# Kernel tuning notes

Measured on AMD Instinct MI355X. Metric: run time of the kernel, lower is better.

## Reference

```python
import jax, jax.numpy as jnp
import numpy as np

N = 50000      # entities
R = 400        # relations
D = 300        # init/hidden/output dim (hard-coded 300 in module)
E = 800000     # edges over N+R nodes
B = 2048       # aligned train pairs
L = 32         # padded neighbor sequence length
H, DK = 8, 32  # n_head=8, d_k=d_v=32
GAMMA1, GAMMA2 = 0.9, 0.2


def setup_inputs() -> dict:
    key = jax.random.key(0)
    ks = iter(jax.random.split(key, 48))
    nk = lambda: next(ks)
    inp = {}
    inp["e_x"] = jax.random.normal(nk(), (N, D), jnp.float32)
    inp["r_x"] = jax.random.normal(nk(), (R, 2 * D), jnp.float32)
    inp["edge_w"] = jax.random.uniform(nk(), (E,), jnp.float32)
    # learned params (fan-in scaled)
    s = lambda fi: 1.0 / np.sqrt(fi)
    inp["Wrel"] = jax.random.normal(nk(), (2 * D, D), jnp.float32) * s(2 * D)
    inp["brel"] = jnp.zeros((D,), jnp.float32)
    inp["W1"] = jax.random.normal(nk(), (D, D), jnp.float32) * s(D)
    inp["b1"] = jnp.zeros((D,), jnp.float32)
    inp["W2"] = jax.random.normal(nk(), (D, D), jnp.float32) * s(D)
    inp["b2"] = jnp.zeros((D,), jnp.float32)
    inp["Wprox"] = jax.random.normal(nk(), (2 * D, D), jnp.float32) * s(2 * D)
    inp["bprox"] = jnp.zeros((D,), jnp.float32)
    # encoder params, index 0 = input_encoder, 1 = output_encoder
    inp["enc_Wq"] = jax.random.normal(nk(), (2, D, H * DK), jnp.float32) * s(D)
    inp["enc_Wk"] = jax.random.normal(nk(), (2, D, H * DK), jnp.float32) * s(D)
    inp["enc_Wv"] = jax.random.normal(nk(), (2, D, H * DK), jnp.float32) * s(D)
    inp["enc_Wo"] = jax.random.normal(nk(), (2, H * DK, D), jnp.float32) * s(H * DK)
    # graph structure
    inp["edge_src"] = jax.random.randint(nk(), (E,), 0, N + R, jnp.int32)
    inp["edge_dst"] = jax.random.randint(nk(), (E,), 0, N + R, jnp.int32)
    # aligned entity pairs + padded neighbor (relation, head) sequences
    inp["l_ids"] = jax.random.randint(nk(), (B,), 0, N, jnp.int32)
    inp["r_ids"] = jax.random.randint(nk(), (B,), 0, N, jnp.int32)
    for p in ("l_in", "l_out", "r_in", "r_out"):
        inp[p + "_rel"] = jax.random.randint(nk(), (B, L), 0, R, jnp.int32)
        inp[p + "_head"] = jax.random.randint(nk(), (B, L), 0, N, jnp.int32)
        inp[p + "_mask"] = jax.random.randint(nk(), (B, L), 0, 2, jnp.int32).astype(bool)
    inp["train_len"] = B
    return inp


def _cosine(x, y):
    xn = x / jnp.maximum(jnp.linalg.norm(x, axis=1, keepdims=True), 1e-8)
    yn = y / jnp.maximum(jnp.linalg.norm(y, axis=1, keepdims=True), 1e-8)
    return xn @ yn.T


def _encoder(rel_seq, head_seq, mask, kernel, ent_f, rel_f, Wq, Wk, Wv, Wo):
    # neighbor tokens: relation emb + head entity emb    [B, L, D]
    tok = ent_f[head_seq] + rel_f[rel_seq]
    b = tok.shape[0]
    q = (kernel @ Wq).reshape(b, H, DK)                  # kernel entity is the query
    k = (tok @ Wk).reshape(b, L, H, DK)
    v = (tok @ Wv).reshape(b, L, H, DK)
    scores = jnp.einsum('bhd,blhd->bhl', q, k) / np.sqrt(DK)
    scores = jnp.where(mask[:, None, :], scores, -1e9)
    attn = jax.nn.softmax(scores, axis=-1)
    ctx = jnp.einsum('bhl,blhd->bhd', attn, v).reshape(b, H * DK)
    out = ctx @ Wo                                       # [B, D]
    # entities with empty neighbor list -> zero vector (original code path)
    return jnp.where(mask.any(-1)[:, None], out, 0.0)


def _get_proximity(ids, in_rel, in_head, in_mask, out_rel, out_head, out_mask,
                   ent_f, rel_f, enc_Wq, enc_Wk, enc_Wv, enc_Wo, Wprox, bprox):
    kernel = ent_f[ids]                                  # [B, D]
    in_em = _encoder(in_rel, in_head, in_mask, kernel, ent_f, rel_f,
                     enc_Wq[0], enc_Wk[0], enc_Wv[0], enc_Wo[0])
    out_em = _encoder(out_rel, out_head, out_mask, kernel, ent_f, rel_f,
                      enc_Wq[1], enc_Wk[1], enc_Wv[1], enc_Wo[1])
    prox = jnp.concatenate([in_em, out_em], axis=1) @ Wprox + bprox
    return jnp.concatenate([kernel, prox], axis=1)       # [B, 2D]


def reference(e_x, r_x, edge_w, Wrel, brel, W1, b1, W2, b2, Wprox, bprox,
              enc_Wq, enc_Wk, enc_Wv, enc_Wo,
              edge_src, edge_dst, l_ids, r_ids,
              l_in_rel, l_in_head, l_in_mask, l_out_rel, l_out_head, l_out_mask,
              r_in_rel, r_in_head, r_in_mask, r_out_rel, r_out_head, r_out_mask,
              train_len):
    NT = N + R
    # relation_linear then relational GCN over joint entity+relation graph
    r0 = r_x @ Wrel + brel                               # [R, D]
    x = jnp.concatenate([e_x, r0], axis=0)               # [NT, D]
    agg1 = jax.ops.segment_sum(edge_w[:, None] * x[edge_src], edge_dst, num_segments=NT)
    h1 = jax.nn.relu(agg1 @ W1 + b1)
    agg2 = jax.ops.segment_sum(edge_w[:, None] * h1[edge_src], edge_dst, num_segments=NT)
    h2 = agg2 @ W2 + b2
    gcn_ex, gcn_rx = h2[:N], h2[N:]
    # proximity embeddings for left/right aligned entities
    lem = _get_proximity(l_ids, l_in_rel, l_in_head, l_in_mask,
                         l_out_rel, l_out_head, l_out_mask,
                         gcn_ex, gcn_rx, enc_Wq, enc_Wk, enc_Wv, enc_Wo, Wprox, bprox)
    rem = _get_proximity(r_ids, r_in_rel, r_in_head, r_in_mask,
                         r_out_rel, r_out_head, r_out_mask,
                         gcn_ex, gcn_rx, enc_Wq, enc_Wk, enc_Wv, enc_Wo, Wprox, bprox)
    # contrastive alignment loss
    sim = _cosine(lem, rem)                              # [B, B]
    diag = jnp.diagonal(sim)
    pos_part = jnp.mean(jnp.minimum(diag, GAMMA1))
    no_diag = sim - jnp.diag(diag)
    neg_part = jnp.mean(jnp.maximum(no_diag, GAMMA2))
    loss = neg_part - GAMMA2 - pos_part + GAMMA1
    return loss, lem, rem
```

## Files before the change

### kernel.cpp

```cpp
#include <hip/hip_runtime.h>
#include <cstdint>
#include <cstddef>

typedef _Float16 f16;
typedef __attribute__((ext_vector_type(8))) _Float16 half8;
typedef __attribute__((ext_vector_type(4))) float f32x4;

#define NE 50000
#define NR 400
#define DD 300
#define NTOT 50400
#define EE 800000
#define BB 2048
#define LL 32
#define HD 256
#define KP1 320
#define KP2 608

__device__ inline void split2h(float x, f16& hi, f16& lo) {
  f16 h = (f16)x;
  hi = h;
  lo = (f16)(x - (float)h);
}

__global__ void copy_f4_kernel(const float4* __restrict__ src, float4* __restrict__ dst, int n4) {
  int i = blockIdx.x * blockDim.x + threadIdx.x;
  if (i < n4) dst[i] = src[i];
}

__global__ void rel_proj_kernel(const float* __restrict__ r_x, const float* __restrict__ Wrel,
                                const float* __restrict__ brel, float* __restrict__ out) {
  int row = blockIdx.x;
  int c = threadIdx.x;
  if (c >= DD) return;
  float acc = brel[c];
  const float* rr = r_x + (size_t)row * (2 * DD);
  for (int k = 0; k < 2 * DD; ++k) acc += rr[k] * Wrel[(size_t)k * DD + c];
  out[(size_t)row * DD + c] = acc;
}

__global__ void hist_kernel(const int* __restrict__ dst, int* __restrict__ counts) {
  int e = blockIdx.x * blockDim.x + threadIdx.x;
  if (e < EE) atomicAdd(&counts[dst[e]], 1);
}

__global__ __launch_bounds__(1024) void scan_kernel(const int* __restrict__ counts,
                                                    int* __restrict__ row_ptr,
                                                    int* __restrict__ cursor) {
  __shared__ int sums[1024];
  const int n = NTOT;
  int t = threadIdx.x;
  const int chunk = (n + 1023) / 1024;
  int begin = t * chunk;
  int end = begin + chunk; if (end > n) end = n;
  int s = 0;
  for (int i = begin; i < end; ++i) s += counts[i];
  sums[t] = s;
  __syncthreads();
  for (int off = 1; off < 1024; off <<= 1) {
    int v = (t >= off) ? sums[t - off] : 0;
    __syncthreads();
    sums[t] += v;
    __syncthreads();
  }
  int run = sums[t] - s;
  for (int i = begin; i < end; ++i) {
    row_ptr[i] = run; cursor[i] = run;
    run += counts[i];
  }
  if (t == 1023) row_ptr[n] = sums[1023];
}

__global__ void scatter_kernel(const int* __restrict__ dst, const int* __restrict__ src,
                               const float* __restrict__ w, int* __restrict__ cursor,
                               int* __restrict__ src_s, float* __restrict__ w_s) {
  int e = blockIdx.x * blockDim.x + threadIdx.x;
  if (e < EE) {
    int pos = atomicAdd(&cursor[dst[e]], 1);
    src_s[pos] = src[e];
    w_s[pos] = w[e];
  }
}

__global__ void detect_mask_kernel(const unsigned* __restrict__ m0, const unsigned* __restrict__ m1,
                                   const unsigned* __restrict__ m2, const unsigned* __restrict__ m3,
                                   int* __restrict__ flag) {
  int idx = blockIdx.x * blockDim.x + threadIdx.x;
  const int wp = BB * LL / 4;
  if (idx >= 4 * wp) return;
  const unsigned* p = idx < wp ? m0 : idx < 2 * wp ? m1 : idx < 3 * wp ? m2 : m3;
  if (p[idx % wp] > 1u) atomicOr(flag, 1);
}

__global__ void norm_mask_kernel(const void* __restrict__ raw, int* __restrict__ outm,
                                 int* __restrict__ many, const int* __restrict__ flag) {
  int idx = blockIdx.x * blockDim.x + threadIdx.x;
  if (idx >= BB * LL) return;
  int v = (*flag) ? (int)((const unsigned char*)raw)[idx] : ((const int*)raw)[idx];
  v = v ? 1 : 0;
  outm[idx] = v;
  if (v) atomicOr(&many[idx >> 5], 1);
}

__global__ void concat_ids_kernel(const int* __restrict__ a, const int* __restrict__ b,
                                  int* __restrict__ o) {
  int i = blockIdx.x * blockDim.x + threadIdx.x;
  if (i < BB) o[i] = a[i];
  else if (i < 2 * BB) o[i] = b[i - BB];
}

__global__ __launch_bounds__(320) void aggregate_kernel(
    const float* __restrict__ feat, f16* __restrict__ outhi, f16* __restrict__ outlo,
    const int* __restrict__ row_ptr, const int* __restrict__ srcs, const float* __restrict__ ws) {
  int d = blockIdx.x;
  int f = threadIdx.x;
  if (f >= DD) return;
  int beg = row_ptr[d], end = row_ptr[d + 1];
  float acc = 0.f;
  int e = beg;
  for (; e + 8 <= end; e += 8) {
    int s[8]; float wv[8]; float v[8];
#pragma unroll
    for (int u = 0; u < 8; ++u) { s[u] = srcs[e + u]; wv[u] = ws[e + u]; }
#pragma unroll
    for (int u = 0; u < 8; ++u) v[u] = feat[(size_t)s[u] * DD + f];
#pragma unroll
    for (int u = 0; u < 8; ++u) acc += wv[u] * v[u];
  }
  for (; e + 2 <= end; e += 2) {
    int s0 = srcs[e], s1 = srcs[e + 1];
    float w0 = ws[e], w1 = ws[e + 1];
    acc += w0 * feat[(size_t)s0 * DD + f] + w1 * feat[(size_t)s1 * DD + f];
  }
  if (e < end) acc += ws[e] * feat[(size_t)srcs[e] * DD + f];
  f16 hi, lo; split2h(acc, hi, lo);
  outhi[(size_t)d * KP1 + f] = hi;
  outlo[(size_t)d * KP1 + f] = lo;
}

__global__ void pad_zero_kernel(f16* __restrict__ hi, f16* __restrict__ lo, int rows, int ld, int c0) {
  int pw = ld - c0;
  int idx = blockIdx.x * blockDim.x + threadIdx.x;
  if (idx >= rows * pw) return;
  int r = idx / pw, c = c0 + idx % pw;
  hi[(size_t)r * ld + c] = (f16)0.f;
  lo[(size_t)r * ld + c] = (f16)0.f;
}

__global__ __launch_bounds__(256) void transpose_split_kernel(
    const float* __restrict__ in, int insz, f16* __restrict__ outhi, f16* __restrict__ outlo,
    int outsz, int Kreal, int Nn, int Kpad) {
  __shared__ float tile[32][33];
  int z = blockIdx.z;
  int k0 = blockIdx.x * 32, n0 = blockIdx.y * 32;
  int tx = threadIdx.x & 31, ty = threadIdx.x >> 5;
#pragma unroll
  for (int r = 0; r < 4; ++r) {
    int k = k0 + ty + r * 8, n = n0 + tx;
    float v = (k < Kreal && n < Nn) ? in[(size_t)z * insz + (size_t)k * Nn + n] : 0.f;
    tile[ty + r * 8][tx] = v;
  }
  __syncthreads();
#pragma unroll
  for (int r = 0; r < 4; ++r) {
    int n = n0 + ty + r * 8, k = k0 + tx;
    if (n < Nn && k < Kpad) {
      f16 h, l; split2h(tile[tx][ty + r * 8], h, l);
      outhi[(size_t)z * outsz + (size_t)n * Kpad + k] = h;
      outlo[(size_t)z * outsz + (size_t)n * Kpad + k] = l;
    }
  }
}

__global__ __launch_bounds__(256, 2) void mfma_gemm_kernel(
    const f16* __restrict__ Ahi, const f16* __restrict__ Alo, int lda,
    const f16* __restrict__ Bhi, const f16* __restrict__ Blo, int ldb,
    int M, int Nn, int K, const int* __restrict__ g1,
    float* __restrict__ C, int ldc, int coloff,
    const float* __restrict__ bias, int dorelu, const int* __restrict__ rowmask,
    f16* __restrict__ Chi, f16* __restrict__ Clo, int ldc16,
    int npass, int wofuse, int losfuse, double* __restrict__ accum) {
  __shared__ int4 sAh[512], sAl[512], sBh[512], sBl[512];
  const int tid = threadIdx.x;
  const int row0 = blockIdx.y * 128, col0 = blockIdx.x * 128;
  const int wave = tid >> 6, lane = tid & 63;
  const int wrow = (wave >> 1) * 64, wcol = (wave & 1) * 64;
  const int m16 = lane & 15, quad = lane >> 4;

  const int sr = tid >> 2, sc = tid & 3;
  const f16* pah[2]; const f16* pal[2]; bool va[2];
  const f16* pbh[2]; const f16* pbl[2]; bool vb[2];
  int sidx[2];
#pragma unroll
  for (int i = 0; i < 2; ++i) {
    int r = sr + i * 64;
    sidx[i] = r * 4 + (sc ^ ((r >> 1) & 3));
    int grow = row0 + r;
    va[i] = grow < M;
    int ar = va[i] ? (g1 ? g1[grow] : grow) : 0;
    pah[i] = Ahi + (size_t)ar * lda + sc * 8;
    pal[i] = Alo + (size_t)ar * lda + sc * 8;
    int gn = col0 + r;
    vb[i] = gn < Nn;
    int br = vb[i] ? gn : 0;
    pbh[i] = Bhi + (size_t)br * ldb + sc * 8;
    pbl[i] = Blo + (size_t)br * ldb + sc * 8;
  }
  int idxA[4], idxB[4];
#pragma unroll
  for (int f = 0; f < 4; ++f) {
    int r = wrow + f * 16 + m16;
    idxA[f] = r * 4 + (quad ^ ((r >> 1) & 3));
    int n = wcol + f * 16 + m16;
    idxB[f] = n * 4 + (quad ^ ((n >> 1) & 3));
  }
  f32x4 acc[4][4];
#pragma unroll
  for (int i = 0; i < 4; ++i)
#pragma unroll
    for (int j = 0; j < 4; ++j) acc[i][j] = (f32x4){0.f, 0.f, 0.f, 0.f};

  const int4 z4 = {0, 0, 0, 0};
  for (int k0 = 0; k0 < K; k0 += 32) {
#pragma unroll
    for (int i = 0; i < 2; ++i) {
      int4 vh = z4, wh = z4;
      if (va[i]) vh = *(const int4*)(pah[i] + k0);
      if (vb[i]) wh = *(const int4*)(pbh[i] + k0);
      sAh[sidx[i]] = vh; sBh[sidx[i]] = wh;
      if (npass >= 2) {
        int4 vl = z4;
        if (va[i]) vl = *(const int4*)(pal[i] + k0);
        sAl[sidx[i]] = vl;
      }
      if (npass >= 3) {
        int4 wl = z4;
        if (vb[i]) wl = *(const int4*)(pbl[i] + k0);
        sBl[sidx[i]] = wl;
      }
    }
    __syncthreads();
    half8 ah[4], bh[4];
#pragma unroll
    for (int f = 0; f < 4; ++f) {
      ah[f] = *(const half8*)&sAh[idxA[f]];
      bh[f] = *(const half8*)&sBh[idxB[f]];
    }
#pragma unroll
    for (int i = 0; i < 4; ++i)
#pragma unroll
      for (int j = 0; j < 4; ++j)
        acc[i][j] = __builtin_amdgcn_mfma_f32_16x16x32_f16(ah[i], bh[j], acc[i][j], 0, 0, 0);
    if (npass >= 2) {
      half8 al[4];
#pragma unroll
      for (int f = 0; f < 4; ++f) al[f] = *(const half8*)&sAl[idxA[f]];
#pragma unroll
      for (int i = 0; i < 4; ++i)
#pragma unroll
        for (int j = 0; j < 4; ++j)
          acc[i][j] = __builtin_amdgcn_mfma_f32_16x16x32_f16(al[i], bh[j], acc[i][j], 0, 0, 0);
    }
    if (npass >= 3) {
      half8 bl[4];
#pragma unroll
      for (int f = 0; f < 4; ++f) bl[f] = *(const half8*)&sBl[idxB[f]];
#pragma unroll
      for (int i = 0; i < 4; ++i)
#pragma unroll
        for (int j = 0; j < 4; ++j)
          acc[i][j] = __builtin_amdgcn_mfma_f32_16x16x32_f16(ah[i], bl[j], acc[i][j], 0, 0, 0);
    }
    __syncthreads();
  }

  if (losfuse) {
    float negs = 0.f, poss = 0.f;
#pragma unroll
    for (int i = 0; i < 4; ++i)
#pragma unroll
      for (int reg = 0; reg < 4; ++reg) {
        int row = row0 + wrow + i * 16 + quad * 4 + reg;
#pragma unroll
        for (int j = 0; j < 4; ++j) {
          int col = col0 + wcol + j * 16 + m16;
          float s = acc[i][j][reg];
          if (row == col) { negs += 0.2f; poss += fminf(s, 0.9f); }
          else negs += fmaxf(s, 0.2f);
        }
      }
    float* rn_ = (float*)sAh;
    float* rp_ = (float*)sAl;
    rn_[tid] = negs; rp_[tid] = poss;
    __syncthreads();
    for (int off2 = 128; off2; off2 >>= 1) {
      if (tid < off2) { rn_[tid] += rn_[tid + off2]; rp_[tid] += rp_[tid + off2]; }
      __syncthreads();
    }
    if (tid == 0) {
      atomicAdd(&accum[0], (double)rn_[0]);
      atomicAdd(&accum[1], (double)rp_[0]);
    }
    return;
  }

#pragma unroll
  for (int i = 0; i < 4; ++i) {
#pragma unroll
    for (int reg = 0; reg < 4; ++reg) {
      int row = row0 + wrow + i * 16 + quad * 4 + reg;
      if (row >= M) continue;
      if (wofuse) {
        int b = row & 2047, side = (row >> 11) & 1, dir = (row >> 12) & 1;
        bool zero = rowmask[(side * 2 + dir) * BB + b] == 0;
        int orow = side * 2048 + b;
#pragma unroll
        for (int j = 0; j < 4; ++j) {
          int col = col0 + wcol + j * 16 + m16;
          if (col >= Nn) continue;
          if ((col >= 300) != (dir != 0)) continue;
          float v = acc[i][j][reg];
          if (zero) v = 0.f;
          f16 hb, lb; split2h(v, hb, lb);
          Chi[(size_t)orow * ldc16 + col] = hb;
          Clo[(size_t)orow * ldc16 + col] = lb;
        }
        continue;
      }
      bool zero = (rowmask != nullptr) && (rowmask[row] == 0);
#pragma unroll
      for (int j = 0; j < 4; ++j) {
        int col = col0 + wcol + j * 16 + m16;
        if (col >= Nn) continue;
        float v = acc[i][j][reg];
        if (bias) v += bias[col];
        if (dorelu) v = fmaxf(v, 0.f);
        if (zero) v = 0.f;
        if (C) C[(size_t)row * ldc + coloff + col] = v;
        if (Chi) {
          f16 hb, lb; split2h(v, hb, lb);
          Chi[(size_t)row * ldc16 + coloff + col] = hb;
          Clo[(size_t)row * ldc16 + coloff + col] = lb;
        }
      }
    }
  }
}

__global__ __launch_bounds__(256) void attention_kernel(
    const float* __restrict__ qAll, const float* __restrict__ kv,
    const int* __restrict__ h0, const int* __restrict__ r0, const int* __restrict__ m0,
    const int* __restrict__ h1, const int* __restrict__ r1, const int* __restrict__ m1,
    int dirOfs, f16* __restrict__ ctxhi, f16* __restrict__ ctxlo) {
  int b = blockIdx.x;
  int side = blockIdx.y;
  int tid = threadIdx.x;
  const int* hs = side ? h1 : h0;
  const int* rs = side ? r1 : r0;
  const int* msk = side ? m1 : m0;
  __shared__ float qs[256];
  __shared__ float attns[8][33];
  __shared__ int hid[32], rid[32], ms[32];
  qs[tid] = qAll[((size_t)(side * BB + b)) * 512 + dirOfs + tid];
  if (tid < 32) {
    hid[tid] = hs[b * LL + tid];
    rid[tid] = NE + rs[b * LL + tid];
    ms[tid] = msk[b * LL + tid];
  }
  __syncthreads();
  int h = tid >> 5, l = tid & 31;
  const float4* k1 = (const float4*)(kv + (size_t)hid[l] * 512 + h * 32);
  const float4* k2 = (const float4*)(kv + (size_t)rid[l] * 512 + h * 32);
  float s = 0.f;
#pragma unroll
  for (int i = 0; i < 8; ++i) {
    float4 a = k1[i], c4 = k2[i];
    const float* qp = &qs[h * 32 + i * 4];
    s += qp[0] * (a.x + c4.x) + qp[1] * (a.y + c4.y) + qp[2] * (a.z + c4.z) + qp[3] * (a.w + c4.w);
  }
  s *= 0.17677669529663687f;
  s = ms[l] ? s : -1e9f;
  float m = s;
  for (int off = 16; off; off >>= 1) m = fmaxf(m, __shfl_xor(m, off, 32));
  float e = expf(s - m);
  float sum = e;
  for (int off = 16; off; off >>= 1) sum += __shfl_xor(sum, off, 32);
  attns[h][l] = e / sum;
  __syncthreads();
  int d = tid & 31;
  float c = 0.f;
#pragma unroll 4
  for (int l2 = 0; l2 < 32; ++l2) {
    float a = attns[h][l2];
    float v = kv[(size_t)hid[l2] * 512 + 256 + h * 32 + d] +
              kv[(size_t)rid[l2] * 512 + 256 + h * 32 + d];
    c += a * v;
  }
  f16 hb, lb; split2h(c, hb, lb);
  size_t o = ((size_t)side * BB + b) * 256 + tid;
  ctxhi[o] = hb;
  ctxlo[o] = lb;
}

__global__ void gather_part_kernel(const f16* __restrict__ enthi, const f16* __restrict__ entlo,
                                   const int* __restrict__ ids, float* __restrict__ out) {
  int b = blockIdx.x;
  int t = threadIdx.x;
  if (t < DD) {
    size_t o = (size_t)ids[b] * KP1 + t;
    out[(size_t)b * 600 + t] = (float)enthi[o] + (float)entlo[o];
  }
}

__global__ __launch_bounds__(256) void rownorm_kernel(const float* __restrict__ rows,
                                                      f16* __restrict__ outhi,
                                                      f16* __restrict__ outlo) {
  int b = blockIdx.x;
  int t = threadIdx.x;
  const float* rp = rows + (size_t)b * 600;
  float s = 0.f;
  for (int c = t; c < 600; c += 256) { float v = rp[c]; s += v * v; }
  __shared__ float red[256];
  red[t] = s;
  __syncthreads();
  for (int off = 128; off; off >>= 1) {
    if (t < off) red[t] += red[t + off];
    __syncthreads();
  }
  __shared__ float inv;
  if (t == 0) inv = 1.f / fmaxf(sqrtf(red[0]), 1e-8f);
  __syncthreads();
  for (int c = t; c < KP2; c += 256) {
    float v = (c < 600) ? rp[c] * inv : 0.f;
    f16 hb, lb; split2h(v, hb, lb);
    outhi[(size_t)b * KP2 + c] = hb;
    outlo[(size_t)b * KP2 + c] = lb;
  }
}

__global__ void finalize_kernel(const double* __restrict__ accum, float* __restrict__ out) {
  double neg = accum[0] / ((double)BB * (double)BB);
  double pos = accum[1] / (double)BB;
  out[0] = (float)(neg - 0.2 - pos + 0.9);
}

static inline void launch_mfma(hipStream_t st, const f16* Ahi, const f16* Alo, int lda,
                               const f16* Bhi, const f16* Blo, int ldb, int M, int Nn, int K,
                               const int* g1, float* C, int ldc, int coloff, const float* bias,
                               int dorelu, const int* rowmask, f16* Chi, f16* Clo, int ldc16,
                               int npass = 3, int wofuse = 0, int losfuse = 0,
                               double* accum = nullptr) {
  dim3 grid((Nn + 127) / 128, (M + 127) / 128);
  mfma_gemm_kernel<<<grid, 256, 0, st>>>(Ahi, Alo, lda, Bhi, Blo, ldb, M, Nn, K, g1, C, ldc,
                                         coloff, bias, dorelu, rowmask, Chi, Clo, ldc16, npass,
                                         wofuse, losfuse, accum);
}

static inline void launch_transpose(hipStream_t st, const float* in, int insz, f16* oh, f16* ol,
                                    int outsz, int Kreal, int Nn, int Kpad, int z) {
  dim3 grid((Kpad + 31) / 32, (Nn + 31) / 32, z);
  transpose_split_kernel<<<grid, 256, 0, st>>>(in, insz, oh, ol, outsz, Kreal, Nn, Kpad);
}

extern "C" void kernel_launch(void* const* d_in, const int* in_sizes, int n_in,
                              void* d_out, int out_size, void* d_ws, size_t ws_size,
                              hipStream_t stream) {
  const float* e_x    = (const float*)d_in[0];
  const float* r_x    = (const float*)d_in[1];
  const float* edge_w = (const float*)d_in[2];
  const float* Wrel   = (const float*)d_in[3];
  const float* brel   = (const float*)d_in[4];
  const float* W1     = (const float*)d_in[5];
  const float* b1     = (const float*)d_in[6];
  const float* W2     = (const float*)d_in[7];
  const float* b2     = (const float*)d_in[8];
  const float* Wprox  = (const float*)d_in[9];
  const float* bprox  = (const float*)d_in[10];
  const float* Wq     = (const float*)d_in[11];
  const float* Wk     = (const float*)d_in[12];
  const float* Wv     = (const float*)d_in[13];
  const float* Wo     = (const float*)d_in[14];
  const int* edge_src = (const int*)d_in[15];
  const int* edge_dst = (const int*)d_in[16];
  const int* l_ids    = (const int*)d_in[17];
  const int* r_ids    = (const int*)d_in[18];
  float* out = (float*)d_out;

  char* base = (char*)d_ws;
  size_t off = 0;
  auto nxt = [&](size_t bytes) -> char* {
    char* p = base + off;
    off += (bytes + 63) & ~(size_t)63;
    return p;
  };
  char* R0 = nxt(64512000);
  char* R1 = nxt(64512000);
  char* R2 = nxt(60480000);
  float* qAll  = (float*)nxt(8388608);
  f16* ctxAhi = (f16*)nxt(4194304);
  f16* ctxAlo = (f16*)nxt(4194304);
  f16* emAhi  = (f16*)nxt(4980736);
  f16* emAlo  = (f16*)nxt(4980736);
  f16* lnhi   = (f16*)nxt(2490368);
  f16* lnlo   = (f16*)nxt(2490368);
  f16* rnhi   = (f16*)nxt(2490368);
  f16* rnlo   = (f16*)nxt(2490368);
  f16* qkvhi  = (f16*)nxt(983040);
  f16* qkvlo  = (f16*)nxt(983040);
  f16* w12hi  = (f16*)nxt(384000);
  f16* w12lo  = (f16*)nxt(384000);
  f16* wohi   = (f16*)nxt(307200);
  f16* wolo   = (f16*)nxt(307200);
  f16* wpxhi  = (f16*)nxt(364800);
  f16* wpxlo  = (f16*)nxt(364800);
  double* accum = (double*)nxt(16);
  int* row_ptr  = (int*)nxt(4 * (NTOT + 1));
  int* cursor   = (int*)nxt(4 * NTOT);
  int* counts   = (int*)nxt(4 * NTOT);
  int* src_s    = (int*)nxt(4 * EE);
  float* w_s    = (float*)nxt(4 * EE);
  int* mask_norm = (int*)nxt(4 * 4 * BB * LL);
  int* maskany   = (int*)nxt(4 * 4 * BB);
  int* idsAll    = (int*)nxt(4 * 2 * BB);
  int* flag      = (int*)nxt(64);

  float* xbuf = (float*)R0;
  f16* h2hi = (f16*)R0;  f16* h2lo = h2hi + (size_t)NTOT * KP1;
  f16* agghi = (f16*)R1; f16* agglo = agghi + (size_t)NTOT * KP1;
  float* kvbuf = (float*)R1;
  float* h1 = (float*)R2;

  hipMemsetAsync(counts, 0, NTOT * sizeof(int), stream);
  hipMemsetAsync(maskany, 0, 4 * BB * sizeof(int), stream);
  hipMemsetAsync(flag, 0, sizeof(int), stream);
  hipMemsetAsync(accum, 0, 2 * sizeof(double), stream);

  copy_f4_kernel<<<(3750000 + 255) / 256, 256, 0, stream>>>((const float4*)e_x, (float4*)xbuf,
                                                            3750000);
  rel_proj_kernel<<<NR, 320, 0, stream>>>(r_x, Wrel, brel, xbuf + (size_t)NE * DD);

  hist_kernel<<<(EE + 255) / 256, 256, 0, stream>>>(edge_dst, counts);
  scan_kernel<<<1, 1024, 0, stream>>>(counts, row_ptr, cursor);
  scatter_kernel<<<(EE + 255) / 256, 256, 0, stream>>>(edge_dst, edge_src, edge_w, cursor, src_s,
                                                       w_s);

  detect_mask_kernel<<<256, 256, 0, stream>>>((const unsigned*)d_in[21], (const unsigned*)d_in[24],
                                              (const unsigned*)d_in[27], (const unsigned*)d_in[30],
                                              flag);
  for (int mi = 0; mi < 4; ++mi)
    norm_mask_kernel<<<(BB * LL + 255) / 256, 256, 0, stream>>>(
        d_in[21 + mi * 3], mask_norm + (size_t)mi * BB * LL, maskany + mi * BB, flag);
  concat_ids_kernel<<<(2 * BB + 255) / 256, 256, 0, stream>>>(l_ids, r_ids, idsAll);

  launch_transpose(stream, Wq, 300 * 256, qkvhi + 0 * 81920, qkvlo + 0 * 81920, 81920, 300, 256,
                   KP1, 2);
  launch_transpose(stream, Wk, 0, qkvhi + 2 * 81920, qkvlo + 2 * 81920, 81920, 300, 256, KP1, 1);
  launch_transpose(stream, Wv, 0, qkvhi + 3 * 81920, qkvlo + 3 * 81920, 81920, 300, 256, KP1, 1);
  launch_transpose(stream, Wk + 300 * 256, 0, qkvhi + 4 * 81920, qkvlo + 4 * 81920, 81920, 300,
                   256, KP1, 1);
  launch_transpose(stream, Wv + 300 * 256, 0, qkvhi + 5 * 81920, qkvlo + 5 * 81920, 81920, 300,
                   256, KP1, 1);
  launch_transpose(stream, W1, 0, w12hi, w12lo, 96000, 300, 300, KP1, 1);
  launch_transpose(stream, W2, 0, w12hi + 96000, w12lo + 96000, 96000, 300, 300, KP1, 1);
  launch_transpose(stream, Wo, 256 * 300, wohi, wolo, 76800, 256, 300, 256, 2);
  launch_transpose(stream, Wprox, 0, wpxhi, wpxlo, 182400, 600, 300, KP2, 1);

  pad_zero_kernel<<<(NTOT * 20 + 255) / 256, 256, 0, stream>>>(agghi, agglo, NTOT, KP1, 300);
  pad_zero_kernel<<<(4096 * 8 + 255) / 256, 256, 0, stream>>>(emAhi, emAlo, 4096, KP2, 600);

  aggregate_kernel<<<NTOT, 320, 0, stream>>>(xbuf, agghi, agglo, row_ptr, src_s, w_s);
  launch_mfma(stream, agghi, agglo, KP1, w12hi, w12lo, KP1, NTOT, 300, KP1, nullptr, h1, 300, 0,
              b1, 1, nullptr, nullptr, nullptr, 0, 2);
  aggregate_kernel<<<NTOT, 320, 0, stream>>>(h1, agghi, agglo, row_ptr, src_s, w_s);
  pad_zero_kernel<<<(NTOT * 20 + 255) / 256, 256, 0, stream>>>(h2hi, h2lo, NTOT, KP1, 300);
  launch_mfma(stream, agghi, agglo, KP1, w12hi + 96000, w12lo + 96000, KP1, NTOT, 300, KP1,
              nullptr, nullptr, 0, 0, b2, 0, nullptr, h2hi, h2lo, KP1, 3);

  launch_mfma(stream, h2hi, h2lo, KP1, qkvhi, qkvlo, KP1, 2 * BB, 512, KP1, idsAll, qAll, 512, 0,
              nullptr, 0, nullptr, nullptr, nullptr, 0, 2);

  for (int dir = 0; dir < 2; ++dir) {
    launch_mfma(stream, h2hi, h2lo, KP1, qkvhi + (2 + 2 * dir) * 81920,
                qkvlo + (2 + 2 * dir) * 81920, KP1, NTOT, 512, KP1, nullptr, kvbuf, 512, 0,
                nullptr, 0, nullptr, nullptr, nullptr, 0, 2);
    attention_kernel<<<dim3(BB, 2), 256, 0, stream>>>(
        qAll, kvbuf,
        (const int*)d_in[20 + dir * 3], (const int*)d_in[19 + dir * 3],
        mask_norm + (size_t)(0 * 2 + dir) * BB * LL,
        (const int*)d_in[26 + dir * 3], (const int*)d_in[25 + dir * 3],
        mask_norm + (size_t)(1 * 2 + dir) * BB * LL,
        dir * 256, ctxAhi + (size_t)dir * 2 * BB * 256, ctxAlo + (size_t)dir * 2 * BB * 256);
  }

  launch_mfma(stream, ctxAhi, ctxAlo, 256, wohi, wolo, 256, 4 * BB, 600, 256, nullptr, nullptr,
              0, 0, nullptr, 0, maskany, emAhi, emAlo, KP2, 3, 1);

  float* lem = out + 1;
  float* rem = out + 1 + (size_t)BB * 600;
  launch_mfma(stream, emAhi, emAlo, KP2, wpxhi, wpxlo, KP2, 4096, 300, KP2, nullptr, lem, 600,
              300, bprox, 0, nullptr, nullptr, nullptr, 0, 3);
  gather_part_kernel<<<BB, 320, 0, stream>>>(h2hi, h2lo, l_ids, lem);
  gather_part_kernel<<<BB, 320, 0, stream>>>(h2hi, h2lo, r_ids, rem);

  rownorm_kernel<<<BB, 256, 0, stream>>>(lem, lnhi, lnlo);
  rownorm_kernel<<<BB, 256, 0, stream>>>(rem, rnhi, rnlo);
  launch_mfma(stream, lnhi, lnlo, KP2, rnhi, rnlo, KP2, BB, BB, KP2, nullptr, nullptr, 0, 0,
              nullptr, 0, nullptr, nullptr, nullptr, 0, 1, 0, 1, accum);
  finalize_kernel<<<1, 1, 0, stream>>>(accum, out);
}
```

Measured before the change: 1.409 ms.

## Store GCN inputs, hidden state and K/V in fp16; batch launches

Entity features, the first GCN hidden layer and the K/V projections are now stored as single fp16 values instead of fp32, which halves the bytes read by the gather-heavy aggregation and attention kernels. The two K/V projection GEMMs become one wider GEMM feeding one attention launch that covers both directions. The weight transposes and the four mask-normalisation passes are each merged into a single launch. The cost is lower precision for these intermediates, since they drop the hi/lo split, which may change numerics slightly.

```diff
diff --git a/kernel.cpp b/kernel.cpp
--- a/kernel.cpp
+++ b/kernel.cpp
@@ -4,6 +4,7 @@
 
 typedef _Float16 f16;
 typedef __attribute__((ext_vector_type(8))) _Float16 half8;
+typedef __attribute__((ext_vector_type(4))) _Float16 half4;
 typedef __attribute__((ext_vector_type(4))) float f32x4;
 
 #define NE 50000
@@ -23,20 +24,24 @@
   lo = (f16)(x - (float)h);
 }
 
-__global__ void copy_f4_kernel(const float4* __restrict__ src, float4* __restrict__ dst, int n4) {
+__global__ void convert_f16_kernel(const float4* __restrict__ src, half4* __restrict__ dst,
+                                   int n4) {
   int i = blockIdx.x * blockDim.x + threadIdx.x;
-  if (i < n4) dst[i] = src[i];
+  if (i < n4) {
+    float4 v = src[i];
+    dst[i] = (half4){(f16)v.x, (f16)v.y, (f16)v.z, (f16)v.w};
+  }
 }
 
 __global__ void rel_proj_kernel(const float* __restrict__ r_x, const float* __restrict__ Wrel,
-                                const float* __restrict__ brel, float* __restrict__ out) {
+                                const float* __restrict__ brel, f16* __restrict__ out) {
   int row = blockIdx.x;
   int c = threadIdx.x;
   if (c >= DD) return;
   float acc = brel[c];
   const float* rr = r_x + (size_t)row * (2 * DD);
   for (int k = 0; k < 2 * DD; ++k) acc += rr[k] * Wrel[(size_t)k * DD + c];
-  out[(size_t)row * DD + c] = acc;
+  out[(size_t)row * DD + c] = (f16)acc;
 }
 
 __global__ void hist_kernel(const int* __restrict__ dst, int* __restrict__ counts) {
@@ -92,11 +97,15 @@
   if (p[idx % wp] > 1u) atomicOr(flag, 1);
 }
 
-__global__ void norm_mask_kernel(const void* __restrict__ raw, int* __restrict__ outm,
-                                 int* __restrict__ many, const int* __restrict__ flag) {
+__global__ void norm_mask4_kernel(const void* __restrict__ r0, const void* __restrict__ r1,
+                                  const void* __restrict__ r2, const void* __restrict__ r3,
+                                  int* __restrict__ outm, int* __restrict__ many,
+                                  const int* __restrict__ flag) {
   int idx = blockIdx.x * blockDim.x + threadIdx.x;
-  if (idx >= BB * LL) return;
-  int v = (*flag) ? (int)((const unsigned char*)raw)[idx] : ((const int*)raw)[idx];
+  if (idx >= 4 * BB * LL) return;
+  int mi = idx / (BB * LL), k = idx % (BB * LL);
+  const void* raw = mi == 0 ? r0 : mi == 1 ? r1 : mi == 2 ? r2 : r3;
+  int v = (*flag) ? (int)((const unsigned char*)raw)[k] : ((const int*)raw)[k];
   v = v ? 1 : 0;
   outm[idx] = v;
   if (v) atomicOr(&many[idx >> 5], 1);
@@ -110,7 +119,7 @@
 }
 
 __global__ __launch_bounds__(320) void aggregate_kernel(
-    const float* __restrict__ feat, f16* __restrict__ outhi, f16* __restrict__ outlo,
+    const f16* __restrict__ feat, f16* __restrict__ outhi, f16* __restrict__ outlo,
     const int* __restrict__ row_ptr, const int* __restrict__ srcs, const float* __restrict__ ws) {
   int d = blockIdx.x;
   int f = threadIdx.x;
@@ -123,16 +132,16 @@
 #pragma unroll
     for (int u = 0; u < 8; ++u) { s[u] = srcs[e + u]; wv[u] = ws[e + u]; }
 #pragma unroll
-    for (int u = 0; u < 8; ++u) v[u] = feat[(size_t)s[u] * DD + f];
+    for (int u = 0; u < 8; ++u) v[u] = (float)feat[(size_t)s[u] * DD + f];
 #pragma unroll
     for (int u = 0; u < 8; ++u) acc += wv[u] * v[u];
   }
   for (; e + 2 <= end; e += 2) {
     int s0 = srcs[e], s1 = srcs[e + 1];
     float w0 = ws[e], w1 = ws[e + 1];
-    acc += w0 * feat[(size_t)s0 * DD + f] + w1 * feat[(size_t)s1 * DD + f];
-  }
-  if (e < end) acc += ws[e] * feat[(size_t)srcs[e] * DD + f];
+    acc += w0 * (float)feat[(size_t)s0 * DD + f] + w1 * (float)feat[(size_t)s1 * DD + f];
+  }
+  if (e < end) acc += ws[e] * (float)feat[(size_t)srcs[e] * DD + f];
   f16 hi, lo; split2h(acc, hi, lo);
   outhi[(size_t)d * KP1 + f] = hi;
   outlo[(size_t)d * KP1 + f] = lo;
@@ -144,30 +153,41 @@
   if (idx >= rows * pw) return;
   int r = idx / pw, c = c0 + idx % pw;
   hi[(size_t)r * ld + c] = (f16)0.f;
-  lo[(size_t)r * ld + c] = (f16)0.f;
-}
-
-__global__ __launch_bounds__(256) void transpose_split_kernel(
-    const float* __restrict__ in, int insz, f16* __restrict__ outhi, f16* __restrict__ outlo,
-    int outsz, int Kreal, int Nn, int Kpad) {
+  if (lo) lo[(size_t)r * ld + c] = (f16)0.f;
+}
+
+#define N_TD 11
+struct TDesc {
+  const float* in; f16* oh; f16* ol;
+  int Kreal, Nn, Kpad, tiles_x, tile_base;
+};
+struct TPack { TDesc d[N_TD]; };
+
+__global__ __launch_bounds__(256) void transpose_multi_kernel(TPack p) {
   __shared__ float tile[32][33];
-  int z = blockIdx.z;
-  int k0 = blockIdx.x * 32, n0 = blockIdx.y * 32;
+  int t = blockIdx.x;
+  int e = 0;
+#pragma unroll
+  for (int i = 1; i < N_TD; ++i)
+    if (t >= p.d[i].tile_base) e = i;
+  TDesc dd = p.d[e];
+  int local = t - dd.tile_base;
+  int k0 = (local % dd.tiles_x) * 32, n0 = (local / dd.tiles_x) * 32;
   int tx = threadIdx.x & 31, ty = threadIdx.x >> 5;
 #pragma unroll
   for (int r = 0; r < 4; ++r) {
     int k = k0 + ty + r * 8, n = n0 + tx;
-    float v = (k < Kreal && n < Nn) ? in[(size_t)z * insz + (size_t)k * Nn + n] : 0.f;
+    float v = (k < dd.Kreal && n < dd.Nn) ? dd.in[(size_t)k * dd.Nn + n] : 0.f;
     tile[ty + r * 8][tx] = v;
   }
   __syncthreads();
 #pragma unroll
   for (int r = 0; r < 4; ++r) {
     int n = n0 + ty + r * 8, k = k0 + tx;
-    if (n < Nn && k < Kpad) {
+    if (n < dd.Nn && k < dd.Kpad) {
       f16 h, l; split2h(tile[tx][ty + r * 8], h, l);
-      outhi[(size_t)z * outsz + (size_t)n * Kpad + k] = h;
-      outlo[(size_t)z * outsz + (size_t)n * Kpad + k] = l;
+      dd.oh[(size_t)n * dd.Kpad + k] = h;
+      dd.ol[(size_t)n * dd.Kpad + k] = l;
     }
   }
 }
@@ -340,7 +360,7 @@
         if (Chi) {
           f16 hb, lb; split2h(v, hb, lb);
           Chi[(size_t)row * ldc16 + coloff + col] = hb;
-          Clo[(size_t)row * ldc16 + coloff + col] = lb;
+          if (Clo) Clo[(size_t)row * ldc16 + coloff + col] = lb;
         }
       }
     }
@@ -348,20 +368,23 @@
 }
 
 __global__ __launch_bounds__(256) void attention_kernel(
-    const float* __restrict__ qAll, const float* __restrict__ kv,
-    const int* __restrict__ h0, const int* __restrict__ r0, const int* __restrict__ m0,
-    const int* __restrict__ h1, const int* __restrict__ r1, const int* __restrict__ m1,
-    int dirOfs, f16* __restrict__ ctxhi, f16* __restrict__ ctxlo) {
+    const float* __restrict__ qAll, const f16* __restrict__ kv,
+    const int* __restrict__ h00, const int* __restrict__ r00,
+    const int* __restrict__ h01, const int* __restrict__ r01,
+    const int* __restrict__ h10, const int* __restrict__ r10,
+    const int* __restrict__ h11, const int* __restrict__ r11,
+    const int* __restrict__ mask_norm, f16* __restrict__ ctxhi, f16* __restrict__ ctxlo) {
   int b = blockIdx.x;
-  int side = blockIdx.y;
+  int y = blockIdx.y;
+  int dir = y >> 1, side = y & 1;
   int tid = threadIdx.x;
-  const int* hs = side ? h1 : h0;
-  const int* rs = side ? r1 : r0;
-  const int* msk = side ? m1 : m0;
+  const int* hs = side ? (dir ? h11 : h10) : (dir ? h01 : h00);
+  const int* rs = side ? (dir ? r11 : r10) : (dir ? r01 : r00);
+  const int* msk = mask_norm + (size_t)(side * 2 + dir) * BB * LL;
   __shared__ float qs[256];
   __shared__ float attns[8][33];
   __shared__ int hid[32], rid[32], ms[32];
-  qs[tid] = qAll[((size_t)(side * BB + b)) * 512 + dirOfs + tid];
+  qs[tid] = qAll[((size_t)(side * BB + b)) * 512 + dir * 256 + tid];
   if (tid < 32) {
     hid[tid] = hs[b * LL + tid];
     rid[tid] = NE + rs[b * LL + tid];
@@ -369,14 +392,15 @@
   }
   __syncthreads();
   int h = tid >> 5, l = tid & 31;
-  const float4* k1 = (const float4*)(kv + (size_t)hid[l] * 512 + h * 32);
-  const float4* k2 = (const float4*)(kv + (size_t)rid[l] * 512 + h * 32);
+  const half8* k1 = (const half8*)(kv + (size_t)hid[l] * 1024 + dir * 512 + h * 32);
+  const half8* k2 = (const half8*)(kv + (size_t)rid[l] * 1024 + dir * 512 + h * 32);
   float s = 0.f;
 #pragma unroll
-  for (int i = 0; i < 8; ++i) {
-    float4 a = k1[i], c4 = k2[i];
-    const float* qp = &qs[h * 32 + i * 4];
-    s += qp[0] * (a.x + c4.x) + qp[1] * (a.y + c4.y) + qp[2] * (a.z + c4.z) + qp[3] * (a.w + c4.w);
+  for (int i = 0; i < 4; ++i) {
+    half8 a = k1[i], c8 = k2[i];
+    const float* qp = &qs[h * 32 + i * 8];
+#pragma unroll
+    for (int j = 0; j < 8; ++j) s += qp[j] * ((float)a[j] + (float)c8[j]);
   }
   s *= 0.17677669529663687f;
   s = ms[l] ? s : -1e9f;
@@ -392,12 +416,12 @@
 #pragma unroll 4
   for (int l2 = 0; l2 < 32; ++l2) {
     float a = attns[h][l2];
-    float v = kv[(size_t)hid[l2] * 512 + 256 + h * 32 + d] +
-              kv[(size_t)rid[l2] * 512 + 256 + h * 32 + d];
+    float v = (float)kv[(size_t)hid[l2] * 1024 + dir * 512 + 256 + h * 32 + d] +
+              (float)kv[(size_t)rid[l2] * 1024 + dir * 512 + 256 + h * 32 + d];
     c += a * v;
   }
   f16 hb, lb; split2h(c, hb, lb);
-  size_t o = ((size_t)side * BB + b) * 256 + tid;
+  size_t o = ((size_t)(dir * 2 + side) * BB + b) * 256 + tid;
   ctxhi[o] = hb;
   ctxlo[o] = lb;
 }
@@ -454,12 +478,6 @@
   mfma_gemm_kernel<<<grid, 256, 0, st>>>(Ahi, Alo, lda, Bhi, Blo, ldb, M, Nn, K, g1, C, ldc,
                                          coloff, bias, dorelu, rowmask, Chi, Clo, ldc16, npass,
                                          wofuse, losfuse, accum);
-}
-
-static inline void launch_transpose(hipStream_t st, const float* in, int insz, f16* oh, f16* ol,
-                                    int outsz, int Kreal, int Nn, int Kpad, int z) {
-  dim3 grid((Kpad + 31) / 32, (Nn + 31) / 32, z);
-  transpose_split_kernel<<<grid, 256, 0, st>>>(in, insz, oh, ol, outsz, Kreal, Nn, Kpad);
 }
 
 extern "C" void kernel_launch(void* const* d_in, const int* in_sizes, int n_in,
@@ -524,20 +542,20 @@
   int* idsAll    = (int*)nxt(4 * 2 * BB);
   int* flag      = (int*)nxt(64);
 
-  float* xbuf = (float*)R0;
+  f16* xbuf16 = (f16*)R0;
   f16* h2hi = (f16*)R0;  f16* h2lo = h2hi + (size_t)NTOT * KP1;
   f16* agghi = (f16*)R1; f16* agglo = agghi + (size_t)NTOT * KP1;
-  float* kvbuf = (float*)R1;
-  float* h1 = (float*)R2;
+  f16* kvAll = (f16*)R1;
+  f16* h1f16 = (f16*)R2;
 
   hipMemsetAsync(counts, 0, NTOT * sizeof(int), stream);
   hipMemsetAsync(maskany, 0, 4 * BB * sizeof(int), stream);
   hipMemsetAsync(flag, 0, sizeof(int), stream);
   hipMemsetAsync(accum, 0, 2 * sizeof(double), stream);
 
-  copy_f4_kernel<<<(3750000 + 255) / 256, 256, 0, stream>>>((const float4*)e_x, (float4*)xbuf,
-                                                            3750000);
-  rel_proj_kernel<<<NR, 320, 0, stream>>>(r_x, Wrel, brel, xbuf + (size_t)NE * DD);
+  convert_f16_kernel<<<(3750000 + 255) / 256, 256, 0, stream>>>((const float4*)e_x,
+                                                                (half4*)xbuf16, 3750000);
+  rel_proj_kernel<<<NR, 320, 0, stream>>>(r_x, Wrel, brel, xbuf16 + (size_t)NE * DD);
 
   hist_kernel<<<(EE + 255) / 256, 256, 0, stream>>>(edge_dst, counts);
   scan_kernel<<<1, 1024, 0, stream>>>(counts, row_ptr, cursor);
@@ -547,31 +565,40 @@
   detect_mask_kernel<<<256, 256, 0, stream>>>((const unsigned*)d_in[21], (const unsigned*)d_in[24],
                                               (const unsigned*)d_in[27], (const unsigned*)d_in[30],
                                               flag);
-  for (int mi = 0; mi < 4; ++mi)
-    norm_mask_kernel<<<(BB * LL + 255) / 256, 256, 0, stream>>>(
-        d_in[21 + mi * 3], mask_norm + (size_t)mi * BB * LL, maskany + mi * BB, flag);
+  norm_mask4_kernel<<<(4 * BB * LL + 255) / 256, 256, 0, stream>>>(
+      d_in[21], d_in[24], d_in[27], d_in[30], mask_norm, maskany, flag);
   concat_ids_kernel<<<(2 * BB + 255) / 256, 256, 0, stream>>>(l_ids, r_ids, idsAll);
 
-  launch_transpose(stream, Wq, 300 * 256, qkvhi + 0 * 81920, qkvlo + 0 * 81920, 81920, 300, 256,
-                   KP1, 2);
-  launch_transpose(stream, Wk, 0, qkvhi + 2 * 81920, qkvlo + 2 * 81920, 81920, 300, 256, KP1, 1);
-  launch_transpose(stream, Wv, 0, qkvhi + 3 * 81920, qkvlo + 3 * 81920, 81920, 300, 256, KP1, 1);
-  launch_transpose(stream, Wk + 300 * 256, 0, qkvhi + 4 * 81920, qkvlo + 4 * 81920, 81920, 300,
-                   256, KP1, 1);
-  launch_transpose(stream, Wv + 300 * 256, 0, qkvhi + 5 * 81920, qkvlo + 5 * 81920, 81920, 300,
-                   256, KP1, 1);
-  launch_transpose(stream, W1, 0, w12hi, w12lo, 96000, 300, 300, KP1, 1);
-  launch_transpose(stream, W2, 0, w12hi + 96000, w12lo + 96000, 96000, 300, 300, KP1, 1);
-  launch_transpose(stream, Wo, 256 * 300, wohi, wolo, 76800, 256, 300, 256, 2);
-  launch_transpose(stream, Wprox, 0, wpxhi, wpxlo, 182400, 600, 300, KP2, 1);
+  {
+    TPack p;
+    int tb = 0, idx = 0;
+    auto add = [&](const float* in, f16* oh, f16* ol, int Kreal, int Nn, int Kpad) {
+      int txs = (Kpad + 31) / 32, tys = (Nn + 31) / 32;
+      p.d[idx] = TDesc{in, oh, ol, Kreal, Nn, Kpad, txs, tb};
+      tb += txs * tys;
+      ++idx;
+    };
+    add(Wq,             qkvhi + 0 * 81920, qkvlo + 0 * 81920, 300, 256, KP1);
+    add(Wq + 300 * 256, qkvhi + 1 * 81920, qkvlo + 1 * 81920, 300, 256, KP1);
+    add(Wk,             qkvhi + 2 * 81920, qkvlo + 2 * 81920, 300, 256, KP1);
+    add(Wv,             qkvhi + 3 * 81920, qkvlo + 3 * 81920, 300, 256, KP1);
+    add(Wk + 300 * 256, qkvhi + 4 * 81920, qkvlo + 4 * 81920, 300, 256, KP1);
+    add(Wv + 300 * 256, qkvhi + 5 * 81920, qkvlo + 5 * 81920, 300, 256, KP1);
+    add(W1,             w12hi,             w12lo,             300, 300, KP1);
+    add(W2,             w12hi + 96000,     w12lo + 96000,     300, 300, KP1);
+    add(Wo,             wohi,              wolo,              256, 300, 256);
+    add(Wo + 256 * 300, wohi + 76800,      wolo + 76800,      256, 300, 256);
+    add(Wprox,          wpxhi,             wpxlo,             600, 300, KP2);
+    transpose_multi_kernel<<<tb, 256, 0, stream>>>(p);
+  }
 
   pad_zero_kernel<<<(NTOT * 20 + 255) / 256, 256, 0, stream>>>(agghi, agglo, NTOT, KP1, 300);
   pad_zero_kernel<<<(4096 * 8 + 255) / 256, 256, 0, stream>>>(emAhi, emAlo, 4096, KP2, 600);
 
-  aggregate_kernel<<<NTOT, 320, 0, stream>>>(xbuf, agghi, agglo, row_ptr, src_s, w_s);
-  launch_mfma(stream, agghi, agglo, KP1, w12hi, w12lo, KP1, NTOT, 300, KP1, nullptr, h1, 300, 0,
-              b1, 1, nullptr, nullptr, nullptr, 0, 2);
-  aggregate_kernel<<<NTOT, 320, 0, stream>>>(h1, agghi, agglo, row_ptr, src_s, w_s);
+  aggregate_kernel<<<NTOT, 320, 0, stream>>>(xbuf16, agghi, agglo, row_ptr, src_s, w_s);
+  launch_mfma(stream, agghi, agglo, KP1, w12hi, w12lo, KP1, NTOT, 300, KP1, nullptr, nullptr, 0,
+              0, b1, 1, nullptr, h1f16, nullptr, 300, 2);
+  aggregate_kernel<<<NTOT, 320, 0, stream>>>(h1f16, agghi, agglo, row_ptr, src_s, w_s);
   pad_zero_kernel<<<(NTOT * 20 + 255) / 256, 256, 0, stream>>>(h2hi, h2lo, NTOT, KP1, 300);
   launch_mfma(stream, agghi, agglo, KP1, w12hi + 96000, w12lo + 96000, KP1, NTOT, 300, KP1,
               nullptr, nullptr, 0, 0, b2, 0, nullptr, h2hi, h2lo, KP1, 3);
@@ -579,18 +606,16 @@
   launch_mfma(stream, h2hi, h2lo, KP1, qkvhi, qkvlo, KP1, 2 * BB, 512, KP1, idsAll, qAll, 512, 0,
               nullptr, 0, nullptr, nullptr, nullptr, 0, 2);
 
-  for (int dir = 0; dir < 2; ++dir) {
-    launch_mfma(stream, h2hi, h2lo, KP1, qkvhi + (2 + 2 * dir) * 81920,
-                qkvlo + (2 + 2 * dir) * 81920, KP1, NTOT, 512, KP1, nullptr, kvbuf, 512, 0,
-                nullptr, 0, nullptr, nullptr, nullptr, 0, 2);
-    attention_kernel<<<dim3(BB, 2), 256, 0, stream>>>(
-        qAll, kvbuf,
-        (const int*)d_in[20 + dir * 3], (const int*)d_in[19 + dir * 3],
-        mask_norm + (size_t)(0 * 2 + dir) * BB * LL,
-        (const int*)d_in[26 + dir * 3], (const int*)d_in[25 + dir * 3],
-        mask_norm + (size_t)(1 * 2 + dir) * BB * LL,
-        dir * 256, ctxAhi + (size_t)dir * 2 * BB * 256, ctxAlo + (size_t)dir * 2 * BB * 256);
-  }
+  launch_mfma(stream, h2hi, h2lo, KP1, qkvhi + 2 * 81920, qkvlo + 2 * 81920, KP1, NTOT, 1024,
+              KP1, nullptr, nullptr, 0, 0, nullptr, 0, nullptr, kvAll, nullptr, 1024, 2);
+
+  attention_kernel<<<dim3(BB, 4), 256, 0, stream>>>(
+      qAll, kvAll,
+      (const int*)d_in[20], (const int*)d_in[19],
+      (const int*)d_in[23], (const int*)d_in[22],
+      (const int*)d_in[26], (const int*)d_in[25],
+      (const int*)d_in[29], (const int*)d_in[28],
+      mask_norm, ctxAhi, ctxAlo);
 
   launch_mfma(stream, ctxAhi, ctxAlo, 256, wohi, wolo, 256, 4 * BB, 600, 256, nullptr, nullptr,
               0, 0, nullptr, 0, maskany, emAhi, emAlo, KP2, 3, 1);
```

Result: faster. 1.174 ms (-16.6%).
